# Kernel optimization log

Measured on AMD Instinct MI355X. Metric: run time of the kernel, lower is better.

Reference implementation:

```python
import jax, jax.numpy as jnp
from jax import lax
import numpy as np

B, D, H, W = 1, 20, 96, 96
N = B * (D - 4) * H * W  # one 7x7x7 guide patch per output voxel
DN = ('NCDHW', 'OIDHW', 'NCDHW')


def _conv3(x, w, b):
    # Conv3d(1,1,kernel=3,stride=1,VALID) + bias
    y = lax.conv_general_dilated(x, w, (1, 1, 1), 'VALID', dimension_numbers=DN)
    return y + b[None, :, None, None, None]


def _guide_branch(x, w1, b1, w2, b2):
    # nn.Sequential(Conv3d, ReLU, Conv3d, ReLU): 7^3 -> 5^3 -> 3^3
    return jax.nn.relu(_conv3(jax.nn.relu(_conv3(x, w1, b1)), w2, b2))


def setup_inputs() -> dict:
    key = jax.random.key(0)
    ks = jax.random.split(key, 12)
    s = 1.0 / np.sqrt(27.0)  # torch Conv3d default init scale (fan_in = 1*3*3*3)
    return {
        'x': jax.random.normal(ks[0], (B, 1, D, H, W), jnp.float32),
        'domain_neighbor': jax.random.uniform(ks[1], (1, 1, 7, 7, 7), jnp.float32),
        'guide_im': jax.random.normal(ks[2], (N, 1, 7, 7, 7), jnp.float32),
        'w1_d': jax.random.normal(ks[3], (1, 1, 3, 3, 3), jnp.float32) * s,
        'b1_d': jax.random.normal(ks[4], (1,), jnp.float32) * s,
        'w2_d': jax.random.normal(ks[5], (1, 1, 3, 3, 3), jnp.float32) * s,
        'b2_d': jax.random.normal(ks[6], (1,), jnp.float32) * s,
        'w1_r': jax.random.normal(ks[7], (1, 1, 3, 3, 3), jnp.float32) * s,
        'b1_r': jax.random.normal(ks[8], (1,), jnp.float32) * s,
        'w2_r': jax.random.normal(ks[9], (1, 1, 3, 3, 3), jnp.float32) * s,
        'b2_r': jax.random.normal(ks[10], (1,), jnp.float32) * s,
    }


def reference(x, domain_neighbor, guide_im, w1_d, b1_d, w2_d, b2_d,
              w1_r, b1_r, w2_r, b2_r):
    Bx, _, Dx, Hx, Wx = x.shape
    # kernel-generating guide nets
    domain_kernel = _guide_branch(domain_neighbor, w1_d, b1_d, w2_d, b2_d)  # (1,1,3,3,3)
    range_kernel = _guide_branch(guide_im, w1_r, b1_r, w2_r, b2_r)          # (N,1,3,3,3)
    weights = (domain_kernel * range_kernel + 1e-10).reshape(-1, 27)        # (N,27)
    # pad H,W by 1 (depth unpadded), extract all 3x3x3 patches (feature order d,h,w)
    xp = jnp.pad(x, ((0, 0), (0, 0), (0, 0), (1, 1), (1, 1)))
    p = lax.conv_general_dilated_patches(xp, (3, 3, 3), (1, 1, 1), 'VALID',
                                         dimension_numbers=DN)  # (B,27,D-2,H,W)
    p = p[:, :, 1:-1]  # keep the D-4 center-aligned depth windows (matches mat_size)
    p = p.transpose(0, 2, 3, 4, 1).reshape(-1, 27)  # (N,27)
    out = jnp.sum(weights * p, axis=1) / jnp.sum(weights, axis=1)  # weighted local mean
    return out.reshape(Bx, 1, Dx - 4, Hx, Wx)
```

## Files before the change

### kernel.cpp

```cpp
#include <hip/hip_runtime.h>
#include <hip/hip_fp16.h>


#define NPATCH 147456
#define TPB     256
#define PPB      64
#define NBLK   (NPATCH / PPB)
#define ROW_H     8
#define PATCH_H 392
#define PATCH_D 196
#define NF4    5488

__global__ __launch_bounds__(128) void domain_branch_kernel(
    const float* __restrict__ dn,
    const float* __restrict__ w1, const float* __restrict__ b1,
    const float* __restrict__ w2, const float* __restrict__ b2,
    float* __restrict__ dom_out)
{
    __shared__ float s_in[344];
    __shared__ float s_c1[128];
    const int t = threadIdx.x;
    for (int idx = t; idx < 343; idx += 128) s_in[idx] = dn[idx];
    __syncthreads();
    if (t < 125) {
        const int i = t / 25, j = (t / 5) % 5, k = t % 5;
        float acc = b1[0];
        const float* base = &s_in[i * 49 + j * 7 + k];
#pragma unroll
        for (int dz = 0; dz < 3; ++dz)
#pragma unroll
            for (int dy = 0; dy < 3; ++dy)
#pragma unroll
                for (int dx = 0; dx < 3; ++dx)
                    acc = fmaf(base[dz * 49 + dy * 7 + dx], w1[dz * 9 + dy * 3 + dx], acc);
        s_c1[t] = fmaxf(acc, 0.f);
    }
    __syncthreads();
    if (t < 27) {
        const int dz = t / 9, dy = (t / 3) % 3, dx = t % 3;
        float acc = b2[0];
#pragma unroll
        for (int u = 0; u < 3; ++u)
#pragma unroll
            for (int v = 0; v < 3; ++v)
#pragma unroll
                for (int q = 0; q < 3; ++q)
                    acc = fmaf(s_c1[(dz + u) * 25 + (dy + v) * 5 + (dx + q)],
                               w2[u * 9 + v * 3 + q], acc);
        dom_out[t] = fmaxf(acc, 0.f);
    }
}

__device__ __forceinline__ float h2f_lo(unsigned int q) {
    return __half2float(__ushort_as_half((unsigned short)(q & 0xffffu)));
}
__device__ __forceinline__ float h2f_hi(unsigned int q) {
    return __half2float(__ushort_as_half((unsigned short)(q >> 16)));
}
__device__ __forceinline__ unsigned short f2h(float f) {
    return __half_as_ushort(__float2half(f));
}

__device__ __forceinline__ void load_row(const unsigned int* __restrict__ P, float* d,
                                         int zi, int y) {
    const int d0 = zi * 28 + y * 4;
    const uint4 q = *reinterpret_cast<const uint4*>(P + d0);
    d[0] = h2f_lo(q.x); d[1] = h2f_hi(q.x);
    d[2] = h2f_lo(q.y); d[3] = h2f_hi(q.y);
    d[4] = h2f_lo(q.z); d[5] = h2f_hi(q.z);
    d[6] = h2f_lo(q.w);
}

template<int IB, int JB, int IE, int JE>
__device__ __forceinline__ void run_tasks(const unsigned int* __restrict__ P,
                                          const float* __restrict__ w1, float bb1,
                                          const float* __restrict__ w2,
                                          float (&a2)[3][3][3])
{
#pragma unroll
    for (int i = IB; i <= IE; ++i) {
        float rw[3][3][7];
        const int j0 = (i == IB) ? JB : 0;
        const int j1 = (i == IE) ? JE : 4;
#pragma unroll
        for (int j = j0; j <= j1; ++j) {
            if (j == j0) {
#pragma unroll
                for (int u = 0; u < 3; ++u)
#pragma unroll
                    for (int dy = 0; dy < 3; ++dy)
                        load_row(P, rw[u][(j + dy) % 3], i + u, j + dy);
            } else {
#pragma unroll
                for (int u = 0; u < 3; ++u)
                    load_row(P, rw[u][(j + 2) % 3], i + u, j + 2);
            }

            float c1r[5];
#pragma unroll
            for (int k = 0; k < 5; ++k) {
                float a = bb1;
#pragma unroll
                for (int u = 0; u < 3; ++u)
#pragma unroll
                    for (int v = 0; v < 3; ++v) {
                        const float* rr = rw[u][(j + v) % 3];
#pragma unroll
                        for (int w = 0; w < 3; ++w)
                            a = fmaf(rr[k + w], w1[u * 9 + v * 3 + w], a);
                    }
                c1r[k] = fmaxf(a, 0.f);
            }

#pragma unroll
            for (int dz2 = 0; dz2 < 3; ++dz2) {
                const int u2 = i - dz2;
                if (u2 >= 0 && u2 < 3) {
#pragma unroll
                    for (int v2 = 0; v2 < 3; ++v2) {
                        const int dy2 = j - v2;
                        if (dy2 >= 0 && dy2 < 3) {
#pragma unroll
                            for (int dx2 = 0; dx2 < 3; ++dx2)
#pragma unroll
                                for (int q = 0; q < 3; ++q)
                                    a2[dz2][dy2][dx2] =
                                        fmaf(c1r[dx2 + q],
                                             w2[u2 * 9 + v2 * 3 + q],
                                             a2[dz2][dy2][dx2]);
                        }
                    }
                }
            }
        }
    }
}

__global__ __launch_bounds__(TPB, 3) void jbf_main_kernel(
    const float* __restrict__ guide, const float* __restrict__ x,
    const float* __restrict__ w1, const float* __restrict__ b1,
    const float* __restrict__ w2, const float* __restrict__ b2,
    const float* __restrict__ dom, float* __restrict__ out)
{
    union SM {
        unsigned short tile[PPB * PATCH_H];
        float part[3][PPB][27];
    };
    __shared__ SM sm;

    const int tid  = threadIdx.x;
    const int wid  = tid >> 6;
    const int lane = tid & 63;
    const int blk  = blockIdx.x;

    const float4* __restrict__ src =
        reinterpret_cast<const float4*>(guide + (size_t)blk * (PPB * 343));

#define STORE4(IT, C) do {                                       \
        int flat = (IT) * (TPB * 4) + tid * 4;                   \
        int p    = flat / 343;                                   \
        int e    = flat - p * 343;                               \
        int r    = e / 7;                                        \
        int xx_  = e - r * 7;                                    \
        int dst  = p * PATCH_H + r * ROW_H + xx_;                \
        float v4[4] = {(C).x, (C).y, (C).z, (C).w};              \
        _Pragma("unroll")                                        \
        for (int el = 0; el < 4; ++el) {                         \
            sm.tile[dst] = f2h(v4[el]);                          \
            ++dst; if (++xx_ == 7) { xx_ = 0; ++dst; }           \
        }                                                        \
    } while (0)

    {
        float4 buf[4];
#pragma unroll
        for (int k = 0; k < 4; ++k) buf[k] = src[k * TPB + tid];

#pragma unroll 1
        for (int it0 = 0; it0 < 20; it0 += 4) {
#pragma unroll
            for (int k = 0; k < 4; ++k) {
                float4 cur = buf[k];
                int idx = (it0 + 4 + k) * TPB + tid;
                if (idx > NF4 - 1) idx = NF4 - 1;
                buf[k] = src[idx];
                STORE4(it0 + k, cur);
            }
        }
        STORE4(20, buf[0]);
        if (tid < 112) STORE4(21, buf[1]);
    }
#undef STORE4
    __syncthreads();

    const unsigned int* __restrict__ P =
        reinterpret_cast<const unsigned int*>(sm.tile) + lane * PATCH_D;
    const float bb1 = b1[0];

    float a2[3][3][3];
    {
        const float init = (wid == 0) ? b2[0] : 0.f;
#pragma unroll
        for (int a = 0; a < 3; ++a)
#pragma unroll
            for (int b = 0; b < 3; ++b)
#pragma unroll
                for (int c = 0; c < 3; ++c) a2[a][b][c] = init;
    }

    if      (wid == 0) run_tasks<0, 0, 1, 1>(P, w1, bb1, w2, a2);
    else if (wid == 1) run_tasks<1, 2, 2, 3>(P, w1, bb1, w2, a2);
    else if (wid == 2) run_tasks<2, 4, 3, 4>(P, w1, bb1, w2, a2);
    else               run_tasks<4, 0, 4, 4>(P, w1, bb1, w2, a2);

    __syncthreads();

    if (wid != 0) {
#pragma unroll
        for (int t = 0; t < 27; ++t)
            sm.part[wid - 1][lane][t] = a2[t / 9][(t / 3) % 3][t % 3];
    }
    __syncthreads();

    if (wid == 0) {
        const int n   = blk * PPB + lane;
        const int dd  = n / 9216;
        const int rem = n - dd * 9216;
        const int h   = rem / 96;
        const int w_  = rem - h * 96;

        float num = 0.f, den = 0.f;
#pragma unroll
        for (int dz = 0; dz < 3; ++dz)
#pragma unroll
            for (int dy = 0; dy < 3; ++dy)
#pragma unroll
                for (int dx = 0; dx < 3; ++dx) {
                    const int t = dz * 9 + dy * 3 + dx;
                    const float r2 = fmaxf(a2[dz][dy][dx] + sm.part[0][lane][t]
                                           + sm.part[1][lane][t]
                                           + sm.part[2][lane][t], 0.f);
                    const float wt = fmaf(dom[t], r2, 1e-10f);
                    const int yy = h - 1 + dy, xx = w_ - 1 + dx;
                    float xv = 0.f;
                    if (yy >= 0 && yy < 96 && xx >= 0 && xx < 96)
                        xv = x[(dd + 1 + dz) * 9216 + yy * 96 + xx];
                    num = fmaf(wt, xv, num);
                    den += wt;
                }
        out[n] = num / den;
    }
}

extern "C" void kernel_launch(void* const* d_in, const int* in_sizes, int n_in,
                              void* d_out, int out_size, void* d_ws, size_t ws_size,
                              hipStream_t stream) {
    const float* x     = (const float*)d_in[0];
    const float* dn    = (const float*)d_in[1];
    const float* guide = (const float*)d_in[2];
    const float* w1_d  = (const float*)d_in[3];
    const float* b1_d  = (const float*)d_in[4];
    const float* w2_d  = (const float*)d_in[5];
    const float* b2_d  = (const float*)d_in[6];
    const float* w1_r  = (const float*)d_in[7];
    const float* b1_r  = (const float*)d_in[8];
    const float* w2_r  = (const float*)d_in[9];
    const float* b2_r  = (const float*)d_in[10];
    float* out = (float*)d_out;
    float* dom = (float*)d_ws;

    domain_branch_kernel<<<1, 128, 0, stream>>>(dn, w1_d, b1_d, w2_d, b2_d, dom);
    jbf_main_kernel<<<NBLK, TPB, 0, stream>>>(guide, x, w1_r, b1_r, w2_r,
                                              b2_r, dom, out);
}
```

Baseline: 51.36 us.

## Split conv work across five waves, one depth slab each

Raises the block from 4 to 5 waves and gives each wave one full depth slab of the first conv layer, replacing the uneven task ranges. The partial second-layer sums are exchanged through a compacted 64x73 shared buffer that holds only the depth slices each wave contributes. The tile-load loop is re-counted for 320 threads. The aim is more parallelism per block and less per-wave serial work, at the cost of higher register and occupancy pressure per block and a still-serial final reduction in wave 0.

```diff
diff --git a/kernel.cpp b/kernel.cpp
--- a/kernel.cpp
+++ b/kernel.cpp
@@ -3,7 +3,7 @@
 
 
 #define NPATCH 147456
-#define TPB     256
+#define TPB     320
 #define PPB      64
 #define NBLK   (NPATCH / PPB)
 #define ROW_H     8
@@ -71,64 +71,59 @@
     d[6] = h2f_lo(q.w);
 }
 
-template<int IB, int JB, int IE, int JE>
-__device__ __forceinline__ void run_tasks(const unsigned int* __restrict__ P,
-                                          const float* __restrict__ w1, float bb1,
-                                          const float* __restrict__ w2,
-                                          float (&a2)[3][3][3])
+template<int I>
+__device__ __forceinline__ void run_slab(const unsigned int* __restrict__ P,
+                                         const float* __restrict__ w1, float bb1,
+                                         const float* __restrict__ w2,
+                                         float (&a2)[3][3][3])
 {
-#pragma unroll
-    for (int i = IB; i <= IE; ++i) {
-        float rw[3][3][7];
-        const int j0 = (i == IB) ? JB : 0;
-        const int j1 = (i == IE) ? JE : 4;
-#pragma unroll
-        for (int j = j0; j <= j1; ++j) {
-            if (j == j0) {
-#pragma unroll
-                for (int u = 0; u < 3; ++u)
-#pragma unroll
-                    for (int dy = 0; dy < 3; ++dy)
-                        load_row(P, rw[u][(j + dy) % 3], i + u, j + dy);
-            } else {
-#pragma unroll
-                for (int u = 0; u < 3; ++u)
-                    load_row(P, rw[u][(j + 2) % 3], i + u, j + 2);
-            }
-
-            float c1r[5];
-#pragma unroll
-            for (int k = 0; k < 5; ++k) {
-                float a = bb1;
-#pragma unroll
-                for (int u = 0; u < 3; ++u)
-#pragma unroll
-                    for (int v = 0; v < 3; ++v) {
-                        const float* rr = rw[u][(j + v) % 3];
-#pragma unroll
-                        for (int w = 0; w < 3; ++w)
-                            a = fmaf(rr[k + w], w1[u * 9 + v * 3 + w], a);
-                    }
-                c1r[k] = fmaxf(a, 0.f);
-            }
-
-#pragma unroll
-            for (int dz2 = 0; dz2 < 3; ++dz2) {
-                const int u2 = i - dz2;
-                if (u2 >= 0 && u2 < 3) {
-#pragma unroll
-                    for (int v2 = 0; v2 < 3; ++v2) {
-                        const int dy2 = j - v2;
-                        if (dy2 >= 0 && dy2 < 3) {
-#pragma unroll
-                            for (int dx2 = 0; dx2 < 3; ++dx2)
-#pragma unroll
-                                for (int q = 0; q < 3; ++q)
-                                    a2[dz2][dy2][dx2] =
-                                        fmaf(c1r[dx2 + q],
-                                             w2[u2 * 9 + v2 * 3 + q],
-                                             a2[dz2][dy2][dx2]);
-                        }
+    float rw[3][3][7];
+#pragma unroll
+    for (int j = 0; j <= 4; ++j) {
+        if (j == 0) {
+#pragma unroll
+            for (int u = 0; u < 3; ++u)
+#pragma unroll
+                for (int dy = 0; dy < 3; ++dy)
+                    load_row(P, rw[u][dy], I + u, dy);
+        } else {
+#pragma unroll
+            for (int u = 0; u < 3; ++u)
+                load_row(P, rw[u][(j + 2) % 3], I + u, j + 2);
+        }
+
+        float c1r[5];
+#pragma unroll
+        for (int k = 0; k < 5; ++k) {
+            float a = bb1;
+#pragma unroll
+            for (int u = 0; u < 3; ++u)
+#pragma unroll
+                for (int v = 0; v < 3; ++v) {
+                    const float* rr = rw[u][(j + v) % 3];
+#pragma unroll
+                    for (int w = 0; w < 3; ++w)
+                        a = fmaf(rr[k + w], w1[u * 9 + v * 3 + w], a);
+                }
+            c1r[k] = fmaxf(a, 0.f);
+        }
+
+#pragma unroll
+        for (int dz2 = 0; dz2 < 3; ++dz2) {
+            const int u2 = I - dz2;
+            if (u2 >= 0 && u2 < 3) {
+#pragma unroll
+                for (int v2 = 0; v2 < 3; ++v2) {
+                    const int dy2 = j - v2;
+                    if (dy2 >= 0 && dy2 < 3) {
+#pragma unroll
+                        for (int dx2 = 0; dx2 < 3; ++dx2)
+#pragma unroll
+                            for (int q = 0; q < 3; ++q)
+                                a2[dz2][dy2][dx2] =
+                                    fmaf(c1r[dx2 + q],
+                                         w2[u2 * 9 + v2 * 3 + q],
+                                         a2[dz2][dy2][dx2]);
                     }
                 }
             }
@@ -144,7 +139,7 @@
 {
     union SM {
         unsigned short tile[PPB * PATCH_H];
-        float part[3][PPB][27];
+        float part[PPB][73];
     };
     __shared__ SM sm;
 
@@ -177,7 +172,7 @@
         for (int k = 0; k < 4; ++k) buf[k] = src[k * TPB + tid];
 
 #pragma unroll 1
-        for (int it0 = 0; it0 < 20; it0 += 4) {
+        for (int it0 = 0; it0 < 16; it0 += 4) {
 #pragma unroll
             for (int k = 0; k < 4; ++k) {
                 float4 cur = buf[k];
@@ -187,8 +182,8 @@
                 STORE4(it0 + k, cur);
             }
         }
-        STORE4(20, buf[0]);
-        if (tid < 112) STORE4(21, buf[1]);
+        STORE4(16, buf[0]);
+        if (tid < 48) STORE4(17, buf[1]);
     }
 #undef STORE4
     __syncthreads();
@@ -208,17 +203,36 @@
                 for (int c = 0; c < 3; ++c) a2[a][b][c] = init;
     }
 
-    if      (wid == 0) run_tasks<0, 0, 1, 1>(P, w1, bb1, w2, a2);
-    else if (wid == 1) run_tasks<1, 2, 2, 3>(P, w1, bb1, w2, a2);
-    else if (wid == 2) run_tasks<2, 4, 3, 4>(P, w1, bb1, w2, a2);
-    else               run_tasks<4, 0, 4, 4>(P, w1, bb1, w2, a2);
-
-    __syncthreads();
-
-    if (wid != 0) {
-#pragma unroll
-        for (int t = 0; t < 27; ++t)
-            sm.part[wid - 1][lane][t] = a2[t / 9][(t / 3) % 3][t % 3];
+    if      (wid == 0) run_slab<0>(P, w1, bb1, w2, a2);
+    else if (wid == 1) run_slab<1>(P, w1, bb1, w2, a2);
+    else if (wid == 2) run_slab<2>(P, w1, bb1, w2, a2);
+    else if (wid == 3) run_slab<3>(P, w1, bb1, w2, a2);
+    else               run_slab<4>(P, w1, bb1, w2, a2);
+
+    __syncthreads();
+
+    if (wid == 1) {
+#pragma unroll
+        for (int dz = 0; dz < 2; ++dz)
+#pragma unroll
+            for (int q = 0; q < 9; ++q)
+                sm.part[lane][dz * 9 + q] = a2[dz][q / 3][q % 3];
+    } else if (wid == 2) {
+#pragma unroll
+        for (int dz = 0; dz < 3; ++dz)
+#pragma unroll
+            for (int q = 0; q < 9; ++q)
+                sm.part[lane][18 + dz * 9 + q] = a2[dz][q / 3][q % 3];
+    } else if (wid == 3) {
+#pragma unroll
+        for (int dz = 1; dz < 3; ++dz)
+#pragma unroll
+            for (int q = 0; q < 9; ++q)
+                sm.part[lane][45 + (dz - 1) * 9 + q] = a2[dz][q / 3][q % 3];
+    } else if (wid == 4) {
+#pragma unroll
+        for (int q = 0; q < 9; ++q)
+            sm.part[lane][63 + q] = a2[2][q / 3][q % 3];
     }
     __syncthreads();
 
@@ -236,11 +250,14 @@
             for (int dy = 0; dy < 3; ++dy)
 #pragma unroll
                 for (int dx = 0; dx < 3; ++dx) {
-                    const int t = dz * 9 + dy * 3 + dx;
-                    const float r2 = fmaxf(a2[dz][dy][dx] + sm.part[0][lane][t]
-                                           + sm.part[1][lane][t]
-                                           + sm.part[2][lane][t], 0.f);
-                    const float wt = fmaf(dom[t], r2, 1e-10f);
+                    const int t9 = dy * 3 + dx;
+                    float r2 = a2[dz][dy][dx];
+                    if (dz < 2)  r2 += sm.part[lane][dz * 9 + t9];
+                    r2 += sm.part[lane][18 + dz * 9 + t9];
+                    if (dz >= 1) r2 += sm.part[lane][45 + (dz - 1) * 9 + t9];
+                    if (dz == 2) r2 += sm.part[lane][63 + t9];
+                    r2 = fmaxf(r2, 0.f);
+                    const float wt = fmaf(dom[dz * 9 + t9], r2, 1e-10f);
                     const int yy = h - 1 + dy, xx = w_ - 1 + dx;
                     float xv = 0.f;
                     if (yy >= 0 && yy < 96 && xx >= 0 && xx < 96)
```

New measurement: 75.06 us. 1.46x slower.

## Stage guide patches row-wise with packed half conversion and vector LDS stores

Applied to the files above, without the earlier changes.

Changes the global-to-LDS staging of guide patches so each thread loads one whole 7-float row (float4 + float2 + float) and writes it to shared memory as a single 16-byte store. It uses packed round-toward-zero fp16 conversion in place of per-element half stores. This removes the per-element index arithmetic, scalar 2-byte LDS writes and the division-heavy address math. Global loads are now unaligned and less coalesced (28-byte row stride per thread). Launch bounds drop from 3 to 2 blocks per SM, which relaxes register pressure. The conversion rounding changes from round-to-nearest to round-toward-zero.

```diff
diff --git a/kernel.cpp b/kernel.cpp
--- a/kernel.cpp
+++ b/kernel.cpp
@@ -9,7 +9,10 @@
 #define ROW_H     8
 #define PATCH_H 392
 #define PATCH_D 196
-#define NF4    5488
+#define NROWS  (PPB * 49)
+
+typedef float f4u __attribute__((ext_vector_type(4), aligned(4)));
+typedef float f2u __attribute__((ext_vector_type(2), aligned(4)));
 
 __global__ __launch_bounds__(128) void domain_branch_kernel(
     const float* __restrict__ dn,
@@ -57,8 +60,8 @@
 __device__ __forceinline__ float h2f_hi(unsigned int q) {
     return __half2float(__ushort_as_half((unsigned short)(q >> 16)));
 }
-__device__ __forceinline__ unsigned short f2h(float f) {
-    return __half_as_ushort(__float2half(f));
+__device__ __forceinline__ unsigned int pkh(float lo, float hi) {
+    return __builtin_bit_cast(unsigned int, __builtin_amdgcn_cvt_pkrtz(lo, hi));
 }
 
 __device__ __forceinline__ void load_row(const unsigned int* __restrict__ P, float* d,
@@ -136,7 +139,7 @@
     }
 }
 
-__global__ __launch_bounds__(TPB, 3) void jbf_main_kernel(
+__global__ __launch_bounds__(TPB, 2) void jbf_main_kernel(
     const float* __restrict__ guide, const float* __restrict__ x,
     const float* __restrict__ w1, const float* __restrict__ b1,
     const float* __restrict__ w2, const float* __restrict__ b2,
@@ -153,44 +156,40 @@
     const int lane = tid & 63;
     const int blk  = blockIdx.x;
 
-    const float4* __restrict__ src =
-        reinterpret_cast<const float4*>(guide + (size_t)blk * (PPB * 343));
-
-#define STORE4(IT, C) do {                                       \
-        int flat = (IT) * (TPB * 4) + tid * 4;                   \
-        int p    = flat / 343;                                   \
-        int e    = flat - p * 343;                               \
-        int r    = e / 7;                                        \
-        int xx_  = e - r * 7;                                    \
-        int dst  = p * PATCH_H + r * ROW_H + xx_;                \
-        float v4[4] = {(C).x, (C).y, (C).z, (C).w};              \
-        _Pragma("unroll")                                        \
-        for (int el = 0; el < 4; ++el) {                         \
-            sm.tile[dst] = f2h(v4[el]);                          \
-            ++dst; if (++xx_ == 7) { xx_ = 0; ++dst; }           \
-        }                                                        \
-    } while (0)
-
     {
-        float4 buf[4];
-#pragma unroll
-        for (int k = 0; k < 4; ++k) buf[k] = src[k * TPB + tid];
+        const float* __restrict__ srcf = guide + (size_t)blk * (PPB * 343);
+        unsigned int* __restrict__ tdw = reinterpret_cast<unsigned int*>(sm.tile);
+
+        int idx = tid;
+        int cp = idx / 49, cr = idx - cp * 49;
+        f4u a = *reinterpret_cast<const f4u*>(srcf + cp * 343 + cr * 7);
+        f2u b = *reinterpret_cast<const f2u*>(srcf + cp * 343 + cr * 7 + 4);
+        float c = srcf[cp * 343 + cr * 7 + 6];
 
 #pragma unroll 1
-        for (int it0 = 0; it0 < 20; it0 += 4) {
-#pragma unroll
-            for (int k = 0; k < 4; ++k) {
-                float4 cur = buf[k];
-                int idx = (it0 + 4 + k) * TPB + tid;
-                if (idx > NF4 - 1) idx = NF4 - 1;
-                buf[k] = src[idx];
-                STORE4(it0 + k, cur);
-            }
+        for (int rd = 0; rd < 12; ++rd) {
+            int nidx = idx + TPB;
+            if (nidx > NROWS - 1) nidx = NROWS - 1;
+            const int np = nidx / 49, nr = nidx - np * 49;
+            const float* s = srcf + np * 343 + nr * 7;
+            f4u na = *reinterpret_cast<const f4u*>(s);
+            f2u nb = *reinterpret_cast<const f2u*>(s + 4);
+            float nc = s[6];
+
+            uint4 q;
+            q.x = pkh(a.x, a.y); q.y = pkh(a.z, a.w);
+            q.z = pkh(b.x, b.y); q.w = pkh(c, 0.f);
+            *reinterpret_cast<uint4*>(tdw + cp * PATCH_D + cr * 4) = q;
+
+            idx = nidx; cp = np; cr = nr; a = na; b = nb; c = nc;
         }
-        STORE4(20, buf[0]);
-        if (tid < 112) STORE4(21, buf[1]);
-    }
-#undef STORE4
+        if (tid < NROWS - 12 * TPB) {
+            uint4 q;
+            q.x = pkh(a.x, a.y); q.y = pkh(a.z, a.w);
+            q.z = pkh(b.x, b.y); q.w = pkh(c, 0.f);
+            *reinterpret_cast<uint4*>(tdw + cp * PATCH_D + cr * 4) = q;
+        }
+    }
     __syncthreads();
 
     const unsigned int* __restrict__ P =
```

New measurement: 52.80 us. 1.03x slower.
